# Kernel tuning notes

Measured on AMD Instinct MI355X. Metric: run time of the kernel, lower is better.

The kernel has to match this reference:

```python
import jax, jax.numpy as jnp
import numpy as np

N, D, E, EDGE_DIM = 8192, 64, 262144, 4


def setup_inputs() -> dict:
    key = jax.random.key(0)
    k1, k2, k3, k4, k5, k6 = jax.random.split(key, 6)
    mag = jax.random.uniform(k1, (N, D), dtype=jnp.float32)
    phase = jax.random.normal(k2, (N, D), dtype=jnp.float32)
    edge_index = jax.random.randint(k3, (2, E), 0, N, dtype=jnp.int64)
    edge_attr = jax.random.normal(k4, (E, EDGE_DIM), dtype=jnp.float32)
    # nn.Linear(edge_dim, hidden_dim): weight [hidden_dim, edge_dim], bias [hidden_dim]
    bound = 1.0 / np.sqrt(EDGE_DIM)
    W = jax.random.uniform(k5, (D, EDGE_DIM), minval=-bound, maxval=bound, dtype=jnp.float32)
    b = jax.random.uniform(k6, (D,), minval=-bound, maxval=bound, dtype=jnp.float32)
    return {"mag": mag, "phase": phase, "edge_index": edge_index,
            "edge_attr": edge_attr, "W": W, "b": b}


def reference(mag, phase, edge_index, edge_attr, W, b):
    # score_ij = sum_d mag_i[d]*mag_j[d]*cos(phase_i[d]-phase_j[d])
    # Via cos(a-b) = cos a cos b + sin a sin b -> two [N,D]@[D,N] matmuls,
    # avoiding the O(N^2 D) intermediate while computing identical math.
    c = mag * jnp.cos(phase)  # [N, D]
    s = mag * jnp.sin(phase)  # [N, D]
    scores = c @ c.T + s @ s.T  # [N, N]
    # edge bias: edge_bias[src, dst] = sum_h Linear(edge_attr)[e, h]
    edge_scores = (edge_attr @ W.T + b).sum(axis=-1)  # [E]
    bias = jnp.zeros((mag.shape[0], mag.shape[0]), dtype=scores.dtype)
    bias = bias.at[edge_index[0], edge_index[1]].set(edge_scores)
    scores = scores + bias
    attn = jax.nn.softmax(scores, axis=1)  # [N, N]
    new_mag = attn @ mag  # [N, D]
    new_phase = attn @ phase  # [N, D]
    return new_mag, new_phase
```

## Files before the change

kernel.cpp:

```cpp
#include <hip/hip_runtime.h>
#include <hip/hip_bf16.h>
#include <cstdint>

#define N_NODES 8192
#define DDIM    64
#define DX      128
#define NEDGE   262144
#define BR      128
#define BC      64
#define SPLITS  8
#define TILES   (N_NODES / BC / SPLITS)
#define RCAP    64
#define MSHIFT  66.0f

typedef float f32x16 __attribute__((ext_vector_type(16)));
typedef short short8 __attribute__((ext_vector_type(8)));

__device__ __forceinline__ short f2bf(float f) {
    union { float f; uint32_t u; } v; v.f = f;
    uint32_t u = v.u;
    uint32_t r = (u + 0x7FFFu + ((u >> 16) & 1u)) >> 16;
    return (short)r;
}
__device__ __forceinline__ float bf2f(short s) {
    union { uint32_t u; float f; } v;
    v.u = ((uint32_t)(uint16_t)s) << 16;
    return v.f;
}
__device__ __forceinline__ unsigned cvtpk_bf16(float lo, float hi) {
    unsigned r;
    asm("v_cvt_pk_bf16_f32 %0, %1, %2" : "=v"(r) : "v"(lo), "v"(hi));
    return r;
}
__device__ __forceinline__ float bfsum2(unsigned w) {
    return bf2f((short)(w & 0xFFFFu)) + bf2f((short)(w >> 16));
}
__device__ __forceinline__ void gload_lds16(const short* g, short* l) {
    __builtin_amdgcn_global_load_lds(
        (const __attribute__((address_space(1))) unsigned int*)g,
        (__attribute__((address_space(3))) unsigned int*)l, 16, 0, 0);
}

__global__ void cpa_prep_all(const float* __restrict__ mag, const float* __restrict__ phase,
                             const int* __restrict__ ei, const float* __restrict__ ea,
                             const float* __restrict__ W, const float* __restrict__ b,
                             short* __restrict__ Xbf, short* __restrict__ Ybt,
                             float* __restrict__ es, int* __restrict__ cnt,
                             int* __restrict__ keys) {
    __shared__ short tile[64][65];
    __shared__ float wsb[5];
    const int blk = blockIdx.x;
    const int tid = threadIdx.x;
    if (blk < 2048) {
        int idx = blk * 256 + tid;
        int i = idx >> 6, d = idx & 63;
        float m = mag[idx], p = phase[idx];
        Xbf[i * DX + d]      = f2bf(m * __cosf(p));
        Xbf[i * DX + 64 + d] = f2bf(m * __sinf(p));
    } else if (blk < 2304) {
        int bb = blk - 2048;
        int bi = bb >> 1;
        int bc = bb & 1;
        int i0 = bi * 64;
        const float* src = bc ? phase : mag;
        for (int itr = 0; itr < 16; ++itr) {
            int idx = tid + itr * 256;
            int ii = idx >> 6, cc = idx & 63;
            tile[ii][cc] = f2bf(src[(size_t)(i0 + ii) * 64 + cc]);
        }
        __syncthreads();
        for (int itr = 0; itr < 16; ++itr) {
            int idx = tid + itr * 256;
            int cc = idx >> 6, ii = idx & 63;
            Ybt[(size_t)(bc * 64 + cc) * N_NODES + i0 + ii] = tile[ii][cc];
        }
    } else {
        if (tid < 64) {
            float w0 = W[tid * 4 + 0], w1 = W[tid * 4 + 1];
            float w2 = W[tid * 4 + 2], w3 = W[tid * 4 + 3];
            float bb = b[tid];
            #pragma unroll
            for (int o = 32; o > 0; o >>= 1) {
                w0 += __shfl_down(w0, o);
                w1 += __shfl_down(w1, o);
                w2 += __shfl_down(w2, o);
                w3 += __shfl_down(w3, o);
                bb += __shfl_down(bb, o);
            }
            if (tid == 0) { wsb[0] = w0; wsb[1] = w1; wsb[2] = w2; wsb[3] = w3; wsb[4] = bb; }
        }
        __syncthreads();
        int e = (blk - 2304) * 256 + tid;
        float4 a = *(const float4*)(ea + (size_t)e * 4);
        es[e] = __expf(a.x * wsb[0] + a.y * wsb[1] + a.z * wsb[2] + a.w * wsb[3] + wsb[4]);
        int src = ei[e];
        int dst = ei[NEDGE + e];
        int pos = atomicAdd(&cnt[src], 1);
        if (pos < RCAP) keys[src * RCAP + pos] = (dst << 18) | e;
    }
}

__global__ __launch_bounds__(256) void cpa_sortrows(const int* __restrict__ cnt,
                                                    int* __restrict__ keys) {
    int row  = blockIdx.x * 4 + (threadIdx.x >> 6);
    int lane = threadIdx.x & 63;
    int len  = min(cnt[row], RCAP);
    int base = row * RCAP;
    int v = (lane < len) ? keys[base + lane] : 0x7FFFFFFF;

    #pragma unroll
    for (int k = 2; k <= 64; k <<= 1) {
        #pragma unroll
        for (int j = k >> 1; j >= 1; j >>= 1) {
            int p = __shfl_xor(v, j);
            bool asc = (lane & k) == 0;
            bool low = (lane & j) == 0;
            v = (low == asc) ? min(v, p) : max(v, p);
        }
    }
    int nxt = __shfl_down(v, 1);
    bool dead = (lane + 1 < len) && ((v >> 18) == (nxt >> 18));
    if (lane < len) keys[base + lane] = v | (dead ? 0x80000000 : 0);
}

__global__ __launch_bounds__(512, 4) void cpa_flash(
    const short* __restrict__ Xbf, const short* __restrict__ Ybt,
    const float* __restrict__ es, const int* __restrict__ keys,
    const int* __restrict__ cnt,
    float* __restrict__ lsplit, short* __restrict__ Opart)
{
    __shared__ short XjT[2][64][128];
    __shared__ short Yt[128][64];
    __shared__ unsigned swp[4][2][2][64][4];

    const int tid  = threadIdx.x;
    const int lane = tid & 63;
    const int w    = tid >> 6;
    const int l31  = lane & 31;
    const int lh   = lane >> 5;
    const int ig   = w >> 1;
    const int jg   = w & 1;

    const int ib = blockIdx.x;
    const int split = blockIdx.y;
    const int i0 = ib * BR;
    const int jstart = split * (N_NODES / SPLITS);

    short8 xi[8];
    #pragma unroll
    for (int kf = 0; kf < 8; ++kf)
        xi[kf] = *(const short8*)(Xbf + (size_t)(i0 + ig * 32 + l31) * DX + kf * 16 + lh * 8);

    const int xr0 = w * 8 + (lane >> 4);
    const int xc  = lane & 15;
    const int xo0 = (xc ^ (xr0 & 15)) << 3;
    const int xr1 = xr0 + 4;
    const int xo1 = (xc ^ (xr1 & 15)) << 3;
    const int yr0 = w * 16 + (lane >> 3);
    const int yc  = lane & 7;
    const int yo0 = (yc ^ (yr0 & 7)) << 3;
    const int yr1 = yr0 + 8;
    const int yo1 = (yc ^ (yr1 & 7)) << 3;

    {
        const short* xsrc = Xbf + (size_t)jstart * DX;
        gload_lds16(xsrc + (size_t)xr0 * DX + xo0, &XjT[0][w * 8][0]);
        gload_lds16(xsrc + (size_t)xr1 * DX + xo1, &XjT[0][w * 8 + 4][0]);
    }

    const int myrow = i0 + ig * 32 + l31;
    int cur  = myrow * RCAP;
    int rend = cur + min(cnt[myrow], RCAP);
    int kcur = 0;
    while (cur < rend) {
        kcur = keys[cur];
        if (((kcur >> 18) & 0x1FFF) >= jstart) break;
        ++cur;
    }

    f32x16 O0, O1;
    float lacc = 0.f;
    #pragma unroll
    for (int r = 0; r < 16; ++r) { O0[r] = 0.f; O1[r] = 0.f; }

    __syncthreads();

    int buf = 0;
    for (int tt = 0; tt < TILES; ++tt) {
        const int j0 = jstart + tt * BC;

        gload_lds16(Ybt + (size_t)yr0 * N_NODES + j0 + yo0, &Yt[w * 16][0]);
        gload_lds16(Ybt + (size_t)yr1 * N_NODES + j0 + yo1, &Yt[w * 16 + 8][0]);
        if (tt + 1 < TILES) {
            const short* xsrc = Xbf + (size_t)(j0 + BC) * DX;
            gload_lds16(xsrc + (size_t)xr0 * DX + xo0, &XjT[buf ^ 1][w * 8][0]);
            gload_lds16(xsrc + (size_t)xr1 * DX + xo1, &XjT[buf ^ 1][w * 8 + 4][0]);
        }

        f32x16 S;
        #pragma unroll
        for (int r = 0; r < 16; ++r) S[r] = 0.f;
        const int rr = jg * 32 + l31;
        __builtin_amdgcn_s_setprio(1);
        #pragma unroll
        for (int kf = 0; kf < 8; ++kf) {
            const int co = kf * 2 + lh;
            short8 af = *(const short8*)&XjT[buf][rr][(co ^ (rr & 15)) << 3];
            S = __builtin_amdgcn_mfma_f32_32x32x16_bf16(af, xi[kf], S, 0, 0, 0);
        }
        __builtin_amdgcn_s_setprio(0);

        f32x16 p;
        #pragma unroll
        for (int r = 0; r < 16; ++r) p[r] = __expf(S[r] - MSHIFT);

        {
            const int wlo  = j0 + jg * 32;
            const int wend = wlo + 32;
            while (cur < rend) {
                int dst = (kcur >> 18) & 0x1FFF;
                if (dst >= wend) break;
                int kk = kcur;
                ++cur;
                if (cur < rend) kcur = keys[cur];
                int jl = dst - wlo;
                if (kk >= 0 && jl >= 0 && ((jl >> 2) & 1) == lh) {
                    float m = es[kk & 0x3FFFF];
                    int sel = (jl & 3) | ((jl >> 3) << 2);
                    #pragma unroll
                    for (int r = 0; r < 16; ++r)
                        if (r == sel) p[r] *= m;
                }
            }
        }

        unsigned c0 = cvtpk_bf16(p[0], p[1]),   c1 = cvtpk_bf16(p[2], p[3]);
        unsigned c2 = cvtpk_bf16(p[4], p[5]),   c3 = cvtpk_bf16(p[6], p[7]);
        unsigned c4 = cvtpk_bf16(p[8], p[9]),   c5 = cvtpk_bf16(p[10], p[11]);
        unsigned c6 = cvtpk_bf16(p[12], p[13]), c7 = cvtpk_bf16(p[14], p[15]);
        unsigned t0 = __shfl_xor(c0, 32), t2 = __shfl_xor(c2, 32);
        unsigned t1 = __shfl_xor(c1, 32), t3 = __shfl_xor(c3, 32);
        unsigned t4 = __shfl_xor(c4, 32), t6 = __shfl_xor(c6, 32);
        unsigned t5 = __shfl_xor(c5, 32), t7 = __shfl_xor(c7, 32);
        union FU { unsigned u[4]; short8 s; int4 v; };
        FU F0, F1;
        F0.u[0] = lh ? t2 : c0;  F0.u[1] = lh ? t3 : c1;
        F0.u[2] = lh ? c2 : t0;  F0.u[3] = lh ? c3 : t1;
        F1.u[0] = lh ? t6 : c4;  F1.u[1] = lh ? t7 : c5;
        F1.u[2] = lh ? c6 : t4;  F1.u[3] = lh ? c7 : t5;

        lacc += bfsum2(F0.u[0]) + bfsum2(F0.u[1]) + bfsum2(F0.u[2]) + bfsum2(F0.u[3]);
        lacc += bfsum2(F1.u[0]) + bfsum2(F1.u[1]) + bfsum2(F1.u[2]) + bfsum2(F1.u[3]);

        *(int4*)&swp[ig][jg][0][lane][0] = F0.v;
        *(int4*)&swp[ig][jg][1][lane][0] = F1.v;

        __syncthreads();

        short8 own0 = F0.s, own1 = F1.s;
        short8 oth0 = *(const short8*)&swp[ig][jg ^ 1][0][lane][0];
        short8 oth1 = *(const short8*)&swp[ig][jg ^ 1][1][lane][0];

        const int fA = jg * 64 + l31;
        const int fB = fA + 32;
        __builtin_amdgcn_s_setprio(1);
        #pragma unroll
        for (int sl = 0; sl < 2; ++sl) {
            short8 ao = sl ? own1 : own0;
            short8 at = sl ? oth1 : oth0;
            const int co_o = jg * 4 + sl * 2 + lh;
            const int co_t = (jg ^ 1) * 4 + sl * 2 + lh;
            short8 b0o = *(const short8*)&Yt[fA][(co_o ^ (fA & 7)) << 3];
            short8 b0t = *(const short8*)&Yt[fA][(co_t ^ (fA & 7)) << 3];
            short8 b1o = *(const short8*)&Yt[fB][(co_o ^ (fB & 7)) << 3];
            short8 b1t = *(const short8*)&Yt[fB][(co_t ^ (fB & 7)) << 3];
            O0 = __builtin_amdgcn_mfma_f32_32x32x16_bf16(ao, b0o, O0, 0, 0, 0);
            O0 = __builtin_amdgcn_mfma_f32_32x32x16_bf16(at, b0t, O0, 0, 0, 0);
            O1 = __builtin_amdgcn_mfma_f32_32x32x16_bf16(ao, b1o, O1, 0, 0, 0);
            O1 = __builtin_amdgcn_mfma_f32_32x32x16_bf16(at, b1t, O1, 0, 0, 0);
        }
        __builtin_amdgcn_s_setprio(0);

        __syncthreads();
        buf ^= 1;
    }

    lacc += __shfl_xor(lacc, 32);
    float* lmbuf = (float*)&swp[0][0][0][0][0];
    if (jg == 1 && lane < 32) lmbuf[ig * 32 + l31] = lacc;
    __syncthreads();
    if (jg == 0 && lane < 32)
        lsplit[(size_t)split * N_NODES + i0 + ig * 32 + l31] = lacc + lmbuf[ig * 32 + l31];

    #pragma unroll
    for (int r = 0; r < 16; ++r) {
        int row = ig * 32 + 4 * lh + (r & 3) + 8 * (r >> 2);
        size_t base = ((size_t)split * N_NODES + i0 + row) * DX;
        Opart[base + jg * 64 + l31]      = f2bf(O0[r]);
        Opart[base + jg * 64 + 32 + l31] = f2bf(O1[r]);
    }
}

__global__ void cpa_merge(const float* __restrict__ lsplit, const short* __restrict__ Opart,
                          float* __restrict__ out) {
    int gid = blockIdx.x * 256 + threadIdx.x;
    int i = gid >> 7;
    int c = gid & 127;
    float den = 0.f, num = 0.f;
    #pragma unroll
    for (int s = 0; s < SPLITS; ++s) {
        den += lsplit[(size_t)s * N_NODES + i];
        num += bf2f(Opart[((size_t)s * N_NODES + i) * DX + c]);
    }
    float val = num / den;
    if (c < 64) out[(size_t)i * 64 + c] = val;
    else        out[(size_t)N_NODES * 64 + (size_t)i * 64 + (c - 64)] = val;
}

extern "C" void kernel_launch(void* const* d_in, const int* in_sizes, int n_in,
                              void* d_out, int out_size, void* d_ws, size_t ws_size,
                              hipStream_t stream)
{
    const float* mag   = (const float*)d_in[0];
    const float* phase = (const float*)d_in[1];
    const int*   ei    = (const int*)d_in[2];
    const float* ea    = (const float*)d_in[3];
    const float* W     = (const float*)d_in[4];
    const float* b     = (const float*)d_in[5];
    float* out = (float*)d_out;

    char* ws = (char*)d_ws;
    short* Xbf    = (short*)(ws + 0);
    short* Ybt    = (short*)(ws + 2097152);
    float* es     = (float*)(ws + 4194304);
    int*   keys   = (int*)  (ws + 5242880);
    int*   cnt    = (int*)  (ws + 7340032);
    float* lsplit = (float*)(ws + 7373056);
    short* Opart  = (short*)(ws + 7635200);

    hipMemsetAsync(cnt, 0, N_NODES * sizeof(int), stream);
    cpa_prep_all<<<2048 + 256 + NEDGE / 256, 256, 0, stream>>>(mag, phase, ei, ea, W, b,
                                                               Xbf, Ybt, es, cnt, keys);
    cpa_sortrows<<<N_NODES / 4, 256, 0, stream>>>(cnt, keys);
    cpa_flash<<<dim3(N_NODES / BR, SPLITS), 512, 0, stream>>>(Xbf, Ybt, es, keys, cnt,
                                                              lsplit, Opart);
    cpa_merge<<<N_NODES * DX / 256, 256, 0, stream>>>(lsplit, Opart, out);
}
```

Before: 169.1 us.

## Load Xj fragments directly from global, double-buffer Y tile, drop cross-lane P shuffle

Permutes the Xbf column layout and the Ybt node order so each lane can read its MFMA A fragments for the key block straight from global memory into registers, and the P fragment no longer needs xor-32 shuffles. The XjT shared tile goes away. Yt and the swap buffer are double-buffered so one barrier per tile replaces two. Exp uses exp2 with a fused multiply-add, the row sum accumulates in fp32 before rounding to bf16, and the grid is reordered so splits vary fastest. The risks are higher global/L2 traffic and register pressure from the per-tile fragment loads.

```diff
diff --git a/kernel.cpp b/kernel.cpp
--- a/kernel.cpp
+++ b/kernel.cpp
@@ -11,7 +11,8 @@
 #define SPLITS  8
 #define TILES   (N_NODES / BC / SPLITS)
 #define RCAP    64
-#define MSHIFT  66.0f
+#define L2E     1.44269504f
+#define MSH2    95.2178727f
 
 typedef float f32x16 __attribute__((ext_vector_type(16)));
 typedef short short8 __attribute__((ext_vector_type(8)));
@@ -31,9 +32,6 @@
     unsigned r;
     asm("v_cvt_pk_bf16_f32 %0, %1, %2" : "=v"(r) : "v"(lo), "v"(hi));
     return r;
-}
-__device__ __forceinline__ float bfsum2(unsigned w) {
-    return bf2f((short)(w & 0xFFFFu)) + bf2f((short)(w >> 16));
 }
 __device__ __forceinline__ void gload_lds16(const short* g, short* l) {
     __builtin_amdgcn_global_load_lds(
@@ -55,8 +53,9 @@
         int idx = blk * 256 + tid;
         int i = idx >> 6, d = idx & 63;
         float m = mag[idx], p = phase[idx];
-        Xbf[i * DX + d]      = f2bf(m * __cosf(p));
-        Xbf[i * DX + 64 + d] = f2bf(m * __sinf(p));
+        int c = ((d >> 3) & 1) * 64 + (d >> 4) * 8 + (d & 7);
+        Xbf[i * DX + c]      = f2bf(m * __cosf(p));
+        Xbf[i * DX + c + 32] = f2bf(m * __sinf(p));
     } else if (blk < 2304) {
         int bb = blk - 2048;
         int bi = bb >> 1;
@@ -72,7 +71,8 @@
         for (int itr = 0; itr < 16; ++itr) {
             int idx = tid + itr * 256;
             int cc = idx >> 6, ii = idx & 63;
-            Ybt[(size_t)(bc * 64 + cc) * N_NODES + i0 + ii] = tile[ii][cc];
+            int jp = (ii & 51) | ((ii & 4) << 1) | ((ii & 8) >> 1);
+            Ybt[(size_t)(bc * 64 + cc) * N_NODES + i0 + jp] = tile[ii][cc];
         }
     } else {
         if (tid < 64) {
@@ -129,9 +129,8 @@
     const int* __restrict__ cnt,
     float* __restrict__ lsplit, short* __restrict__ Opart)
 {
-    __shared__ short XjT[2][64][128];
-    __shared__ short Yt[128][64];
-    __shared__ unsigned swp[4][2][2][64][4];
+    __shared__ short Yt[2][128][64];
+    __shared__ unsigned swp[2][4][2][2][64][4];
 
     const int tid  = threadIdx.x;
     const int lane = tid & 63;
@@ -141,32 +140,21 @@
     const int ig   = w >> 1;
     const int jg   = w & 1;
 
-    const int ib = blockIdx.x;
-    const int split = blockIdx.y;
+    const int split = blockIdx.x;
+    const int ib    = blockIdx.y;
     const int i0 = ib * BR;
     const int jstart = split * (N_NODES / SPLITS);
 
+    const short* xirow = Xbf + (size_t)(i0 + ig * 32 + l31) * DX + lh * 64;
     short8 xi[8];
     #pragma unroll
     for (int kf = 0; kf < 8; ++kf)
-        xi[kf] = *(const short8*)(Xbf + (size_t)(i0 + ig * 32 + l31) * DX + kf * 16 + lh * 8);
-
-    const int xr0 = w * 8 + (lane >> 4);
-    const int xc  = lane & 15;
-    const int xo0 = (xc ^ (xr0 & 15)) << 3;
-    const int xr1 = xr0 + 4;
-    const int xo1 = (xc ^ (xr1 & 15)) << 3;
-    const int yr0 = w * 16 + (lane >> 3);
-    const int yc  = lane & 7;
-    const int yo0 = (yc ^ (yr0 & 7)) << 3;
-    const int yr1 = yr0 + 8;
-    const int yo1 = (yc ^ (yr1 & 7)) << 3;
-
-    {
-        const short* xsrc = Xbf + (size_t)jstart * DX;
-        gload_lds16(xsrc + (size_t)xr0 * DX + xo0, &XjT[0][w * 8][0]);
-        gload_lds16(xsrc + (size_t)xr1 * DX + xo1, &XjT[0][w * 8 + 4][0]);
-    }
+        xi[kf] = *(const short8*)(xirow + kf * 8);
+
+    const int yr  = w * 16 + (lane >> 3);
+    const int yo  = ((lane & 7) ^ (yr & 7)) << 3;
+    const int yr2 = yr + 8;
+    const int yo2 = ((lane & 7) ^ (yr2 & 7)) << 3;
 
     const int myrow = i0 + ig * 32 + l31;
     int cur  = myrow * RCAP;
@@ -183,36 +171,38 @@
     #pragma unroll
     for (int r = 0; r < 16; ++r) { O0[r] = 0.f; O1[r] = 0.f; }
 
-    __syncthreads();
-
-    int buf = 0;
+    gload_lds16(Ybt + (size_t)yr * N_NODES + jstart + yo,   &Yt[0][w * 16][0]);
+    gload_lds16(Ybt + (size_t)yr2 * N_NODES + jstart + yo2, &Yt[0][w * 16 + 8][0]);
+
     for (int tt = 0; tt < TILES; ++tt) {
         const int j0 = jstart + tt * BC;
-
-        gload_lds16(Ybt + (size_t)yr0 * N_NODES + j0 + yo0, &Yt[w * 16][0]);
-        gload_lds16(Ybt + (size_t)yr1 * N_NODES + j0 + yo1, &Yt[w * 16 + 8][0]);
+        const int b  = tt & 1;
+
+        const short* arow = Xbf + (size_t)(j0 + jg * 32 + l31) * DX + lh * 64;
+        short8 af[8];
+        #pragma unroll
+        for (int kf = 0; kf < 8; ++kf)
+            af[kf] = *(const short8*)(arow + kf * 8);
+        __builtin_amdgcn_sched_barrier(0);
+
         if (tt + 1 < TILES) {
-            const short* xsrc = Xbf + (size_t)(j0 + BC) * DX;
-            gload_lds16(xsrc + (size_t)xr0 * DX + xo0, &XjT[buf ^ 1][w * 8][0]);
-            gload_lds16(xsrc + (size_t)xr1 * DX + xo1, &XjT[buf ^ 1][w * 8 + 4][0]);
+            gload_lds16(Ybt + (size_t)yr * N_NODES + (j0 + BC) + yo,   &Yt[b ^ 1][w * 16][0]);
+            gload_lds16(Ybt + (size_t)yr2 * N_NODES + (j0 + BC) + yo2, &Yt[b ^ 1][w * 16 + 8][0]);
         }
 
         f32x16 S;
         #pragma unroll
         for (int r = 0; r < 16; ++r) S[r] = 0.f;
-        const int rr = jg * 32 + l31;
         __builtin_amdgcn_s_setprio(1);
         #pragma unroll
-        for (int kf = 0; kf < 8; ++kf) {
-            const int co = kf * 2 + lh;
-            short8 af = *(const short8*)&XjT[buf][rr][(co ^ (rr & 15)) << 3];
-            S = __builtin_amdgcn_mfma_f32_32x32x16_bf16(af, xi[kf], S, 0, 0, 0);
-        }
+        for (int kf = 0; kf < 8; ++kf)
+            S = __builtin_amdgcn_mfma_f32_32x32x16_bf16(af[kf], xi[kf], S, 0, 0, 0);
         __builtin_amdgcn_s_setprio(0);
 
         f32x16 p;
         #pragma unroll
-        for (int r = 0; r < 16; ++r) p[r] = __expf(S[r] - MSHIFT);
+        for (int r = 0; r < 16; ++r)
+            p[r] = exp2f(__builtin_fmaf(S[r], L2E, -MSH2));
 
         {
             const int wlo  = j0 + jg * 32;
@@ -234,32 +224,26 @@
             }
         }
 
-        unsigned c0 = cvtpk_bf16(p[0], p[1]),   c1 = cvtpk_bf16(p[2], p[3]);
-        unsigned c2 = cvtpk_bf16(p[4], p[5]),   c3 = cvtpk_bf16(p[6], p[7]);
-        unsigned c4 = cvtpk_bf16(p[8], p[9]),   c5 = cvtpk_bf16(p[10], p[11]);
-        unsigned c6 = cvtpk_bf16(p[12], p[13]), c7 = cvtpk_bf16(p[14], p[15]);
-        unsigned t0 = __shfl_xor(c0, 32), t2 = __shfl_xor(c2, 32);
-        unsigned t1 = __shfl_xor(c1, 32), t3 = __shfl_xor(c3, 32);
-        unsigned t4 = __shfl_xor(c4, 32), t6 = __shfl_xor(c6, 32);
-        unsigned t5 = __shfl_xor(c5, 32), t7 = __shfl_xor(c7, 32);
+        #pragma unroll
+        for (int r = 0; r < 16; ++r) lacc += p[r];
+
         union FU { unsigned u[4]; short8 s; int4 v; };
         FU F0, F1;
-        F0.u[0] = lh ? t2 : c0;  F0.u[1] = lh ? t3 : c1;
-        F0.u[2] = lh ? c2 : t0;  F0.u[3] = lh ? c3 : t1;
-        F1.u[0] = lh ? t6 : c4;  F1.u[1] = lh ? t7 : c5;
-        F1.u[2] = lh ? c6 : t4;  F1.u[3] = lh ? c7 : t5;
-
-        lacc += bfsum2(F0.u[0]) + bfsum2(F0.u[1]) + bfsum2(F0.u[2]) + bfsum2(F0.u[3]);
-        lacc += bfsum2(F1.u[0]) + bfsum2(F1.u[1]) + bfsum2(F1.u[2]) + bfsum2(F1.u[3]);
-
-        *(int4*)&swp[ig][jg][0][lane][0] = F0.v;
-        *(int4*)&swp[ig][jg][1][lane][0] = F1.v;
-
-        __syncthreads();
+        F0.u[0] = cvtpk_bf16(p[0], p[1]);   F0.u[1] = cvtpk_bf16(p[2], p[3]);
+        F0.u[2] = cvtpk_bf16(p[4], p[5]);   F0.u[3] = cvtpk_bf16(p[6], p[7]);
+        F1.u[0] = cvtpk_bf16(p[8], p[9]);   F1.u[1] = cvtpk_bf16(p[10], p[11]);
+        F1.u[2] = cvtpk_bf16(p[12], p[13]); F1.u[3] = cvtpk_bf16(p[14], p[15]);
+
+        *(int4*)&swp[b][ig][jg][0][lane][0] = F0.v;
+        *(int4*)&swp[b][ig][jg][1][lane][0] = F1.v;
+
+        asm volatile("s_waitcnt lgkmcnt(0)" ::: "memory");
+        __builtin_amdgcn_s_barrier();
+        __builtin_amdgcn_sched_barrier(0);
 
         short8 own0 = F0.s, own1 = F1.s;
-        short8 oth0 = *(const short8*)&swp[ig][jg ^ 1][0][lane][0];
-        short8 oth1 = *(const short8*)&swp[ig][jg ^ 1][1][lane][0];
+        short8 oth0 = *(const short8*)&swp[b][ig][jg ^ 1][0][lane][0];
+        short8 oth1 = *(const short8*)&swp[b][ig][jg ^ 1][1][lane][0];
 
         const int fA = jg * 64 + l31;
         const int fB = fA + 32;
@@ -270,23 +254,20 @@
             short8 at = sl ? oth1 : oth0;
             const int co_o = jg * 4 + sl * 2 + lh;
             const int co_t = (jg ^ 1) * 4 + sl * 2 + lh;
-            short8 b0o = *(const short8*)&Yt[fA][(co_o ^ (fA & 7)) << 3];
-            short8 b0t = *(const short8*)&Yt[fA][(co_t ^ (fA & 7)) << 3];
-            short8 b1o = *(const short8*)&Yt[fB][(co_o ^ (fB & 7)) << 3];
-            short8 b1t = *(const short8*)&Yt[fB][(co_t ^ (fB & 7)) << 3];
+            short8 b0o = *(const short8*)&Yt[b][fA][(co_o ^ (fA & 7)) << 3];
+            short8 b0t = *(const short8*)&Yt[b][fA][(co_t ^ (fA & 7)) << 3];
+            short8 b1o = *(const short8*)&Yt[b][fB][(co_o ^ (fB & 7)) << 3];
+            short8 b1t = *(const short8*)&Yt[b][fB][(co_t ^ (fB & 7)) << 3];
             O0 = __builtin_amdgcn_mfma_f32_32x32x16_bf16(ao, b0o, O0, 0, 0, 0);
             O0 = __builtin_amdgcn_mfma_f32_32x32x16_bf16(at, b0t, O0, 0, 0, 0);
             O1 = __builtin_amdgcn_mfma_f32_32x32x16_bf16(ao, b1o, O1, 0, 0, 0);
             O1 = __builtin_amdgcn_mfma_f32_32x32x16_bf16(at, b1t, O1, 0, 0, 0);
         }
         __builtin_amdgcn_s_setprio(0);
-
-        __syncthreads();
-        buf ^= 1;
     }
 
     lacc += __shfl_xor(lacc, 32);
-    float* lmbuf = (float*)&swp[0][0][0][0][0];
+    float* lmbuf = (float*)&swp[0][0][0][0][0][0];
     if (jg == 1 && lane < 32) lmbuf[ig * 32 + l31] = lacc;
     __syncthreads();
     if (jg == 0 && lane < 32)
@@ -338,11 +319,11 @@
     float* lsplit = (float*)(ws + 7373056);
     short* Opart  = (short*)(ws + 7635200);
 
-    hipMemsetAsync(cnt, 0, N_NODES * sizeof(int), stream);
+    (void)hipMemsetAsync(cnt, 0, N_NODES * sizeof(int), stream);
     cpa_prep_all<<<2048 + 256 + NEDGE / 256, 256, 0, stream>>>(mag, phase, ei, ea, W, b,
                                                                Xbf, Ybt, es, cnt, keys);
     cpa_sortrows<<<N_NODES / 4, 256, 0, stream>>>(cnt, keys);
-    cpa_flash<<<dim3(N_NODES / BR, SPLITS), 512, 0, stream>>>(Xbf, Ybt, es, keys, cnt,
+    cpa_flash<<<dim3(SPLITS, N_NODES / BR), 512, 0, stream>>>(Xbf, Ybt, es, keys, cnt,
                                                               lsplit, Opart);
     cpa_merge<<<N_NODES * DX / 256, 256, 0, stream>>>(lsplit, Opart, out);
 }
```

After: 232.7 us. 37.7% more time.
